# Kernel tuning notes

Hardware: AMD Instinct MI355X
Metric: run time of the kernel (lower is better)

The kernel has to match this reference:

```python
import jax, jax.numpy as jnp
import numpy as np


def setup_inputs() -> dict:
    key = jax.random.key(0)
    ks = jax.random.split(key, 5)
    B, NINS, NHID = 128, 4096, 128
    inputs = jax.random.normal(ks[0], (B, NINS, NHID), dtype=jnp.float32)
    claims = jax.random.normal(ks[1], (B, NHID), dtype=jnp.float32)  # unused by forward
    # project: Linear(2*nhid -> 64) -> ReLU -> Linear(64 -> 1)
    W1 = jax.random.normal(ks[2], (2 * NHID, 64), dtype=jnp.float32) * (1.0 / np.sqrt(2 * NHID))
    b1 = jnp.zeros((64,), dtype=jnp.float32)
    W2 = jax.random.normal(ks[3], (64, 1), dtype=jnp.float32) * (1.0 / np.sqrt(64))
    b2 = jnp.zeros((1,), dtype=jnp.float32)
    return {"inputs": inputs, "index": 5, "claims": claims,
            "W1": W1, "b1": b1, "W2": W2, "b2": b2}


def reference(inputs, index, claims, W1, b1, W2, b2):
    # inputs: [B, nins, nhid]
    B, NINS, NHID = inputs.shape
    own = jax.lax.dynamic_slice_in_dim(inputs, index, 1, axis=1)  # [B, 1, nhid]
    own = jnp.broadcast_to(own, (B, NINS, NHID))                  # repeat over nins
    tmp = jnp.concatenate([own, inputs], axis=2)                  # [B, nins, 2*nhid]
    h = jax.nn.relu(jnp.einsum('bnd,dk->bnk', tmp, W1) + b1)      # [B, nins, 64]
    att = jnp.einsum('bnk,ko->bno', h, W2) + b2                   # [B, nins, 1]
    weights = jax.nn.softmax(att[..., 0], axis=1)                 # [B, nins]
    outputs = jnp.einsum('bnd,bn->bd', inputs, weights)           # [B, nhid]
    return outputs
```

## Files before the change

### kernel.cpp

```cpp
#include <hip/hip_runtime.h>
#include <math.h>

#define BATCH 128
#define NINS  4096
#define NHID  128
#define KH    64
#define NPART 64
#define PART_STRIDE 136
#define O_OFF 8
#define TILES_PER_WAVE 4

typedef __attribute__((ext_vector_type(8))) short short8;
typedef __attribute__((ext_vector_type(4))) float f32x4;

__device__ inline unsigned short f2bf(float f) {
    union { float f; unsigned u; } v; v.f = f;
    return (unsigned short)((v.u + 0x7FFFu + ((v.u >> 16) & 1u)) >> 16);
}

__device__ inline void cvt2(short8& f, int j, float a, float b) {
#if __has_builtin(__builtin_amdgcn_cvt_pk_bf16_f32)
    typedef __attribute__((ext_vector_type(2))) __bf16 bf16x2;
    bf16x2 p = __builtin_amdgcn_cvt_pk_bf16_f32(a, b);
    short s[2];
    __builtin_memcpy(s, &p, 4);
    f[j] = s[0]; f[j + 1] = s[1];
#else
    f[j] = (short)f2bf(a); f[j + 1] = (short)f2bf(b);
#endif
}

__global__ void precompute_c(const float* __restrict__ inputs,
                             const int* __restrict__ index_p,
                             const float* __restrict__ W1,
                             const float* __restrict__ b1,
                             float* __restrict__ c) {
    const int b = blockIdx.x;
    const int k = threadIdx.x;
    const int idx = index_p[0];
    const float* own = inputs + ((size_t)b * NINS + idx) * NHID;
    float acc = b1[k];
    #pragma unroll 8
    for (int d = 0; d < NHID; ++d)
        acc = fmaf(own[d], W1[d * KH + k], acc);
    c[b * KH + k] = acc;
}

__global__ __launch_bounds__(256)
void att_partial(const float* __restrict__ inputs,
                 const float* __restrict__ W1,
                 const float* __restrict__ W2,
                 const float* __restrict__ b2_p,
                 const float* __restrict__ c,
                 float* __restrict__ part) {
    __shared__ float ebuf[4][64];
    const int lane = threadIdx.x & 63;
    const int wv   = threadIdx.x >> 6;
    const int b    = blockIdx.y;
    const int quad = lane >> 4;
    const int m16  = lane & 15;

    const float* Wb = W1 + (size_t)NHID * KH;
    const float* xb = inputs + (size_t)b * NINS * NHID;

    short8 Bf[4][4];
    #pragma unroll
    for (int ks = 0; ks < 4; ++ks)
        #pragma unroll
        for (int nf = 0; nf < 4; ++nf) {
            const float* wp = Wb + (size_t)(ks * 32 + quad * 8) * KH + nf * 16 + m16;
            short8 f;
            #pragma unroll
            for (int j = 0; j < 8; j += 2)
                cvt2(f, j, wp[(size_t)j * KH], wp[(size_t)(j + 1) * KH]);
            Bf[ks][nf] = f;
        }

    float w2v[4];
    #pragma unroll
    for (int nf = 0; nf < 4; ++nf) w2v[nf] = W2[nf * 16 + m16];
    const float b2v = b2_p[0];
    float cv[4];
    #pragma unroll
    for (int nf = 0; nf < 4; ++nf) cv[nf] = c[b * KH + nf * 16 + m16];

    for (int t = 0; t < TILES_PER_WAVE; ++t) {
        const int tile = (blockIdx.x * 4 + wv) * TILES_PER_WAVE + t;
        const int n0   = tile * 64;

        f32x4 acc[4][4];
        #pragma unroll
        for (int mf = 0; mf < 4; ++mf)
            #pragma unroll
            for (int nf = 0; nf < 4; ++nf) {
                f32x4 z = {cv[nf], cv[nf], cv[nf], cv[nf]};
                acc[mf][nf] = z;
            }

        #pragma unroll
        for (int ks = 0; ks < 4; ++ks) {
            short8 Af[4];
            #pragma unroll
            for (int mf = 0; mf < 4; ++mf) {
                const float* row = xb + (size_t)(n0 + mf * 16 + m16) * NHID
                                      + ks * 32 + quad * 8;
                f32x4 a  = *(const f32x4*)row;
                f32x4 bq = *(const f32x4*)(row + 4);
                short8 f;
                cvt2(f, 0, a.x,  a.y);
                cvt2(f, 2, a.z,  a.w);
                cvt2(f, 4, bq.x, bq.y);
                cvt2(f, 6, bq.z, bq.w);
                Af[mf] = f;
            }
            #pragma unroll
            for (int mf = 0; mf < 4; ++mf)
                #pragma unroll
                for (int nf = 0; nf < 4; ++nf)
                    acc[mf][nf] = __builtin_amdgcn_mfma_f32_16x16x32_bf16(
                        Af[mf], Bf[ks][nf], acc[mf][nf], 0, 0, 0);
        }

        float att[4][4];
        #pragma unroll
        for (int mf = 0; mf < 4; ++mf)
            #pragma unroll
            for (int r = 0; r < 4; ++r) {
                float s = 0.0f;
                #pragma unroll
                for (int nf = 0; nf < 4; ++nf)
                    s = fmaf(fmaxf(acc[mf][nf][r], 0.0f), w2v[nf], s);
                s += __shfl_xor(s, 1);
                s += __shfl_xor(s, 2);
                s += __shfl_xor(s, 4);
                s += __shfl_xor(s, 8);
                att[mf][r] = s + b2v;
            }

        float mx = att[0][0];
        #pragma unroll
        for (int mf = 0; mf < 4; ++mf)
            #pragma unroll
            for (int r = 0; r < 4; ++r) mx = fmaxf(mx, att[mf][r]);
        mx = fmaxf(mx, __shfl_xor(mx, 16));
        mx = fmaxf(mx, __shfl_xor(mx, 32));

        float ev[4][4];
        float L = 0.0f;
        #pragma unroll
        for (int mf = 0; mf < 4; ++mf)
            #pragma unroll
            for (int r = 0; r < 4; ++r) {
                ev[mf][r] = __expf(att[mf][r] - mx);
                L += ev[mf][r];
            }
        L += __shfl_xor(L, 16);
        L += __shfl_xor(L, 32);

        if (m16 == 0) {
            #pragma unroll
            for (int mf = 0; mf < 4; ++mf)
                #pragma unroll
                for (int r = 0; r < 4; ++r)
                    ebuf[wv][mf * 16 + quad * 4 + r] = ev[mf][r];
        }

        const int G  = lane >> 5;
        const int db = (lane & 31) * 4;
        f32x4 o = {0.0f, 0.0f, 0.0f, 0.0f};
        #pragma unroll
        for (int nn = 0; nn < 32; nn += 8) {
            f32x4 e4a = *(const f32x4*)&ebuf[wv][G * 32 + nn];
            f32x4 e4b = *(const f32x4*)&ebuf[wv][G * 32 + nn + 4];
            const float* xrow0 = xb + (size_t)(n0 + G * 32 + nn) * NHID + db;
            #pragma unroll
            for (int j = 0; j < 4; ++j) {
                f32x4 xv = *(const f32x4*)(xrow0 + (size_t)j * NHID);
                o += xv * e4a[j];
            }
            #pragma unroll
            for (int j = 0; j < 4; ++j) {
                f32x4 xv = *(const f32x4*)(xrow0 + (size_t)(j + 4) * NHID);
                o += xv * e4b[j];
            }
        }
        #pragma unroll
        for (int i = 0; i < 4; ++i) o[i] += __shfl_xor(o[i], 32);

        float* p = part + (size_t)(b * NPART + tile) * PART_STRIDE;
        if (lane == 0) { p[0] = mx; p[1] = L; }
        if (lane < 32) *(f32x4*)(p + O_OFF + db) = o;
    }
}

__global__ void finalize(const float* __restrict__ part,
                         float* __restrict__ out) {
    const int b = blockIdx.x;
    const int d = threadIdx.x;
    const float* pb = part + (size_t)b * NPART * PART_STRIDE;

    float M = pb[0];
    #pragma unroll 8
    for (int p = 1; p < NPART; ++p)
        M = fmaxf(M, pb[p * PART_STRIDE]);

    float S = 0.0f, acc = 0.0f;
    #pragma unroll 4
    for (int p = 0; p < NPART; ++p) {
        const float sc = __expf(pb[p * PART_STRIDE] - M);
        S   = fmaf(sc, pb[p * PART_STRIDE + 1], S);
        acc = fmaf(sc, pb[p * PART_STRIDE + O_OFF + d], acc);
    }
    out[b * NHID + d] = acc / S;
}

extern "C" void kernel_launch(void* const* d_in, const int* in_sizes, int n_in,
                              void* d_out, int out_size, void* d_ws, size_t ws_size,
                              hipStream_t stream) {
    const float* inputs = (const float*)d_in[0];
    const int*   index  = (const int*)  d_in[1];
    const float* W1     = (const float*)d_in[3];
    const float* b1     = (const float*)d_in[4];
    const float* W2     = (const float*)d_in[5];
    const float* b2     = (const float*)d_in[6];
    float* out = (float*)d_out;

    float* c    = (float*)d_ws;
    float* part = c + BATCH * KH;

    precompute_c<<<dim3(BATCH), dim3(64), 0, stream>>>(inputs, index, W1, b1, c);

    dim3 gB(4, BATCH);
    att_partial<<<gB, dim3(256), 0, stream>>>(inputs, W1, W2, b2, c, part);

    finalize<<<dim3(BATCH), dim3(NHID), 0, stream>>>(part, out);
}
```

Baseline: 443.1 us.

## Stage W1 fragments in LDS and halve tile size to raise occupancy

Stores the bf16-converted W1 half in a shared-memory transposed buffer and reloads B fragments from LDS per k-step, instead of keeping all 16 fragments in registers. Tiles shrink from 64 to 32 rows, and each wave handles 2 tiles instead of 4. The grid grows fourfold to 2048 blocks, with launch bounds requesting 4 blocks per SM. The goal is to cut register pressure and expose more parallelism for the memory-bound streaming over inputs. The cost is extra LDS traffic, a block-wide sync for W staging, and twice as many partials for finalize to merge.

```diff
diff --git a/kernel.cpp b/kernel.cpp
--- a/kernel.cpp
+++ b/kernel.cpp
@@ -5,10 +5,10 @@
 #define NINS  4096
 #define NHID  128
 #define KH    64
-#define NPART 64
+#define NPART 128
 #define PART_STRIDE 136
 #define O_OFF 8
-#define TILES_PER_WAVE 4
+#define TPW 2
 
 typedef __attribute__((ext_vector_type(8))) short short8;
 typedef __attribute__((ext_vector_type(4))) float f32x4;
@@ -18,16 +18,19 @@
     return (unsigned short)((v.u + 0x7FFFu + ((v.u >> 16) & 1u)) >> 16);
 }
 
-__device__ inline void cvt2(short8& f, int j, float a, float b) {
+__device__ inline unsigned cvt_pk_u32(float a, float b) {
 #if __has_builtin(__builtin_amdgcn_cvt_pk_bf16_f32)
     typedef __attribute__((ext_vector_type(2))) __bf16 bf16x2;
     bf16x2 p = __builtin_amdgcn_cvt_pk_bf16_f32(a, b);
-    short s[2];
-    __builtin_memcpy(s, &p, 4);
-    f[j] = s[0]; f[j + 1] = s[1];
+    unsigned u; __builtin_memcpy(&u, &p, 4); return u;
 #else
-    f[j] = (short)f2bf(a); f[j + 1] = (short)f2bf(b);
+    return (unsigned)f2bf(a) | ((unsigned)f2bf(b) << 16);
 #endif
+}
+
+__device__ inline void cvt2(short8& f, int j, float a, float b) {
+    unsigned u = cvt_pk_u32(a, b);
+    f[j] = (short)(u & 0xffffu); f[j + 1] = (short)(u >> 16);
 }
 
 __global__ void precompute_c(const float* __restrict__ inputs,
@@ -46,35 +49,36 @@
     c[b * KH + k] = acc;
 }
 
-__global__ __launch_bounds__(256)
+__global__ __launch_bounds__(256, 4)
 void att_partial(const float* __restrict__ inputs,
                  const float* __restrict__ W1,
                  const float* __restrict__ W2,
                  const float* __restrict__ b2_p,
                  const float* __restrict__ c,
                  float* __restrict__ part) {
-    __shared__ float ebuf[4][64];
-    const int lane = threadIdx.x & 63;
-    const int wv   = threadIdx.x >> 6;
+    __shared__ unsigned short WbT[KH][NHID + 8];
+    __shared__ float ebuf[4][32];
+
+    const int tid  = threadIdx.x;
+    const int lane = tid & 63;
+    const int wv   = tid >> 6;
     const int b    = blockIdx.y;
     const int quad = lane >> 4;
     const int m16  = lane & 15;
 
-    const float* Wb = W1 + (size_t)NHID * KH;
     const float* xb = inputs + (size_t)b * NINS * NHID;
 
-    short8 Bf[4][4];
-    #pragma unroll
-    for (int ks = 0; ks < 4; ++ks)
-        #pragma unroll
-        for (int nf = 0; nf < 4; ++nf) {
-            const float* wp = Wb + (size_t)(ks * 32 + quad * 8) * KH + nf * 16 + m16;
-            short8 f;
-            #pragma unroll
-            for (int j = 0; j < 8; j += 2)
-                cvt2(f, j, wp[(size_t)j * KH], wp[(size_t)(j + 1) * KH]);
-            Bf[ks][nf] = f;
-        }
+    {
+        const int n  = tid >> 2;
+        const int kb = (tid & 3) * 32;
+        const float* wp = W1 + (size_t)(NHID + kb) * KH + n;
+        #pragma unroll
+        for (int j = 0; j < 32; j += 2) {
+            unsigned u = cvt_pk_u32(wp[(size_t)j * KH], wp[(size_t)(j + 1) * KH]);
+            *(unsigned*)&WbT[n][kb + j] = u;
+        }
+    }
+    __syncthreads();
 
     float w2v[4];
     #pragma unroll
@@ -84,13 +88,13 @@
     #pragma unroll
     for (int nf = 0; nf < 4; ++nf) cv[nf] = c[b * KH + nf * 16 + m16];
 
-    for (int t = 0; t < TILES_PER_WAVE; ++t) {
-        const int tile = (blockIdx.x * 4 + wv) * TILES_PER_WAVE + t;
-        const int n0   = tile * 64;
-
-        f32x4 acc[4][4];
-        #pragma unroll
-        for (int mf = 0; mf < 4; ++mf)
+    for (int t = 0; t < TPW; ++t) {
+        const int tile = (blockIdx.x * 4 + wv) * TPW + t;
+        const int n0   = tile * 32;
+
+        f32x4 acc[2][4];
+        #pragma unroll
+        for (int mf = 0; mf < 2; ++mf)
             #pragma unroll
             for (int nf = 0; nf < 4; ++nf) {
                 f32x4 z = {cv[nf], cv[nf], cv[nf], cv[nf]};
@@ -99,9 +103,14 @@
 
         #pragma unroll
         for (int ks = 0; ks < 4; ++ks) {
-            short8 Af[4];
-            #pragma unroll
-            for (int mf = 0; mf < 4; ++mf) {
+            short8 Bf[4];
+            #pragma unroll
+            for (int nf = 0; nf < 4; ++nf)
+                Bf[nf] = *(const short8*)&WbT[nf * 16 + m16][ks * 32 + quad * 8];
+
+            short8 Af[2];
+            #pragma unroll
+            for (int mf = 0; mf < 2; ++mf) {
                 const float* row = xb + (size_t)(n0 + mf * 16 + m16) * NHID
                                       + ks * 32 + quad * 8;
                 f32x4 a  = *(const f32x4*)row;
@@ -114,16 +123,16 @@
                 Af[mf] = f;
             }
             #pragma unroll
-            for (int mf = 0; mf < 4; ++mf)
+            for (int mf = 0; mf < 2; ++mf)
                 #pragma unroll
                 for (int nf = 0; nf < 4; ++nf)
                     acc[mf][nf] = __builtin_amdgcn_mfma_f32_16x16x32_bf16(
-                        Af[mf], Bf[ks][nf], acc[mf][nf], 0, 0, 0);
-        }
-
-        float att[4][4];
-        #pragma unroll
-        for (int mf = 0; mf < 4; ++mf)
+                        Af[mf], Bf[nf], acc[mf][nf], 0, 0, 0);
+        }
+
+        float att[2][4];
+        #pragma unroll
+        for (int mf = 0; mf < 2; ++mf)
             #pragma unroll
             for (int r = 0; r < 4; ++r) {
                 float s = 0.0f;
@@ -139,16 +148,16 @@
 
         float mx = att[0][0];
         #pragma unroll
-        for (int mf = 0; mf < 4; ++mf)
+        for (int mf = 0; mf < 2; ++mf)
             #pragma unroll
             for (int r = 0; r < 4; ++r) mx = fmaxf(mx, att[mf][r]);
         mx = fmaxf(mx, __shfl_xor(mx, 16));
         mx = fmaxf(mx, __shfl_xor(mx, 32));
 
-        float ev[4][4];
+        float ev[2][4];
         float L = 0.0f;
         #pragma unroll
-        for (int mf = 0; mf < 4; ++mf)
+        for (int mf = 0; mf < 2; ++mf)
             #pragma unroll
             for (int r = 0; r < 4; ++r) {
                 ev[mf][r] = __expf(att[mf][r] - mx);
@@ -159,7 +168,7 @@
 
         if (m16 == 0) {
             #pragma unroll
-            for (int mf = 0; mf < 4; ++mf)
+            for (int mf = 0; mf < 2; ++mf)
                 #pragma unroll
                 for (int r = 0; r < 4; ++r)
                     ebuf[wv][mf * 16 + quad * 4 + r] = ev[mf][r];
@@ -167,22 +176,17 @@
 
         const int G  = lane >> 5;
         const int db = (lane & 31) * 4;
+        f32x4 e4[4];
+        #pragma unroll
+        for (int i = 0; i < 4; ++i)
+            e4[i] = *(const f32x4*)&ebuf[wv][G * 16 + i * 4];
+
         f32x4 o = {0.0f, 0.0f, 0.0f, 0.0f};
-        #pragma unroll
-        for (int nn = 0; nn < 32; nn += 8) {
-            f32x4 e4a = *(const f32x4*)&ebuf[wv][G * 32 + nn];
-            f32x4 e4b = *(const f32x4*)&ebuf[wv][G * 32 + nn + 4];
-            const float* xrow0 = xb + (size_t)(n0 + G * 32 + nn) * NHID + db;
-            #pragma unroll
-            for (int j = 0; j < 4; ++j) {
-                f32x4 xv = *(const f32x4*)(xrow0 + (size_t)j * NHID);
-                o += xv * e4a[j];
-            }
-            #pragma unroll
-            for (int j = 0; j < 4; ++j) {
-                f32x4 xv = *(const f32x4*)(xrow0 + (size_t)(j + 4) * NHID);
-                o += xv * e4b[j];
-            }
+        const float* xr = xb + (size_t)(n0 + G * 16) * NHID + db;
+        #pragma unroll
+        for (int jj = 0; jj < 16; ++jj) {
+            f32x4 xv = *(const f32x4*)(xr + (size_t)jj * NHID);
+            o += xv * e4[jj >> 2][jj & 3];
         }
         #pragma unroll
         for (int i = 0; i < 4; ++i) o[i] += __shfl_xor(o[i], 32);
@@ -230,7 +234,7 @@
 
     precompute_c<<<dim3(BATCH), dim3(64), 0, stream>>>(inputs, index, W1, b1, c);
 
-    dim3 gB(4, BATCH);
+    dim3 gB(NPART / (4 * TPW), BATCH);
     att_partial<<<gB, dim3(256), 0, stream>>>(inputs, W1, W2, b2, c, part);
 
     finalize<<<dim3(BATCH), dim3(NHID), 0, stream>>>(part, out);
```

Result: faster. 417.7 us (-5.7%).
